# Kernel optimization log

Measured on AMD Instinct MI355X. Metric: run time of the kernel, lower is better.

The kernel has to match this reference:

```python
import jax, jax.numpy as jnp
import numpy as np

B, S, D = 2, 2048, 1024
H = 16
HD = D // H  # 64


def setup_inputs() -> dict:
    key = jax.random.key(0)
    ks = jax.random.split(key, 9)
    s = 1.0 / np.sqrt(D)
    x = jax.random.normal(ks[0], (B, S, D), dtype=jnp.float32)
    Wq = jax.random.normal(ks[1], (D, D), dtype=jnp.float32) * s
    Wk = jax.random.normal(ks[2], (D, D), dtype=jnp.float32) * s
    Wv = jax.random.normal(ks[3], (D, D), dtype=jnp.float32) * s
    Wo = jax.random.normal(ks[4], (D, D), dtype=jnp.float32) * s
    bq = jnp.zeros((D,), jnp.float32)
    bk = jnp.zeros((D,), jnp.float32)
    bv = jnp.zeros((D,), jnp.float32)
    bo = jnp.zeros((D,), jnp.float32)
    # causal mask, broadcastable to (B, H, S, S)
    mask = jnp.tril(jnp.ones((S, S), dtype=bool))[None, None, :, :]
    return {"x": x, "Wq": Wq, "bq": bq, "Wk": Wk, "bk": bk,
            "Wv": Wv, "bv": bv, "Wo": Wo, "bo": bo, "mask": mask}


def _split_heads(t):
    # (B, S, D) -> (B, H, S, HD)
    b, s, _ = t.shape
    return t.reshape(b, s, H, HD).transpose(0, 2, 1, 3)


def reference(x, Wq, bq, Wk, bk, Wv, bv, Wo, bo, mask):
    q = _split_heads(x @ Wq + bq)
    k = _split_heads(x @ Wk + bk)
    v = _split_heads(x @ Wv + bv)
    scale = 1.0 / jnp.sqrt(jnp.asarray(HD, dtype=q.dtype))
    scores = jnp.einsum('bhqd,bhkd->bhqk', q, k) * scale
    large_neg = jnp.finfo(scores.dtype).min
    scores = jnp.where(mask, scores, large_neg)
    attn = jax.nn.softmax(scores, axis=-1)
    out = jnp.einsum('bhqk,bhkd->bhqd', attn, v)  # (B,H,S,HD)
    out = out.transpose(0, 2, 1, 3).reshape(x.shape[0], x.shape[1], D)
    return out @ Wo + bo
```

## Files before the change

kernel.cpp:

```cpp
#include <hip/hip_runtime.h>
#include <hip/hip_bf16.h>

typedef __attribute__((ext_vector_type(8))) short bf16x8;
typedef __attribute__((ext_vector_type(4))) float f32x4;
typedef __attribute__((ext_vector_type(16))) float f32x16;

#define B_DIM  2
#define S_DIM  2048
#define D_DIM  1024
#define H_DIM  16
#define HD_DIM 64

__device__ __forceinline__ float bf2f(ushort u) {
    union { unsigned int ui; float f; } c; c.ui = ((unsigned int)u) << 16; return c.f;
}
__device__ __forceinline__ ushort f2bf(float f) {
    __hip_bfloat16 h = __float2bfloat16(f);
    return *reinterpret_cast<ushort*>(&h);
}

__device__ __forceinline__ void async_cp16(const ushort* g, ushort* l) {
    __builtin_amdgcn_global_load_lds(
        (const __attribute__((address_space(1))) void*)g,
        (__attribute__((address_space(3))) void*)l, 16, 0, 0);
}

__device__ __forceinline__ unsigned int cvt_pk_bf16(float lo, float hi) {
    unsigned int d;
    asm volatile("v_cvt_pk_bf16_f32 %0, %1, %2" : "=v"(d) : "v"(lo), "v"(hi));
    return d;
}
__device__ __forceinline__ void pl32swap(unsigned int& a, unsigned int& b) {
    asm volatile("v_permlane32_swap_b32 %0, %1" : "+v"(a), "+v"(b));
}

__global__ __launch_bounds__(256) void detect_kernel(const ushort* __restrict__ x,
                                                     int* __restrict__ flag) {
    __shared__ int any;
    int tid = threadIdx.x;
    if (tid == 0) any = 0;
    __syncthreads();
    int cnt = 0;
    for (int j = 0; j < 64; ++j) {
        ushort u = x[tid * 64 + j];
        if (((u >> 7) & 0xFF) == 0xFF) cnt++;
    }
    if (cnt) atomicOr(&any, 1);
    __syncthreads();
    if (tid == 0) *flag = any ? 1 : 0;
}

__global__ __launch_bounds__(256) void prep_kernel(const void* __restrict__ x,
                                                   const void* __restrict__ Wq,
                                                   const void* __restrict__ Wk,
                                                   const void* __restrict__ Wv,
                                                   const void* __restrict__ Wo,
                                                   const void* __restrict__ bq,
                                                   const void* __restrict__ bk,
                                                   const void* __restrict__ bv,
                                                   const void* __restrict__ bo,
                                                   ushort* __restrict__ xc,
                                                   ushort* __restrict__ Wqkvt,
                                                   ushort* __restrict__ Wot,
                                                   float* __restrict__ biasf,
                                                   const int* __restrict__ flag) {
    int tid = threadIdx.x;
    int z = blockIdx.z;
    bool isf32 = (*flag != 0);

    if (z == 4) {
        int t = (blockIdx.y * 16 + blockIdx.x) * 256 + tid;
#pragma unroll
        for (int c = 0; c < 8; ++c) {
            int i = t + c * 65536;
            if (isf32) {
                const float* s = (const float*)x;
                f32x4 a = *(const f32x4*)&s[(size_t)i * 8];
                f32x4 b = *(const f32x4*)&s[(size_t)i * 8 + 4];
                bf16x8 o;
                o[0] = f2bf(a.x); o[1] = f2bf(a.y); o[2] = f2bf(a.z); o[3] = f2bf(a.w);
                o[4] = f2bf(b.x); o[5] = f2bf(b.y); o[6] = f2bf(b.z); o[7] = f2bf(b.w);
                *(bf16x8*)&xc[(size_t)i * 8] = o;
            } else {
                *(bf16x8*)&xc[(size_t)i * 8] =
                    *(const bf16x8*)&((const ushort*)x)[(size_t)i * 8];
            }
        }
        return;
    }
    if (z == 5) {
        int bid = blockIdx.y * 16 + blockIdx.x;
        if (bid >= 16) return;
        int i = bid * 256 + tid;
        int w = i >> 10, j = i & 1023;
        const void* s = (w == 0) ? bq : (w == 1) ? bk : (w == 2) ? bv : bo;
        biasf[i] = isf32 ? ((const float*)s)[j] : bf2f(((const ushort*)s)[j]);
        return;
    }

    __shared__ ushort tile[64][72];
    const void* src = (z == 0) ? Wq : (z == 1) ? Wk : (z == 2) ? Wv : Wo;
    ushort* dst = (z < 3) ? (Wqkvt + (size_t)z * D_DIM * D_DIM) : Wot;
    int r0 = blockIdx.y * 64, c0 = blockIdx.x * 64;
#pragma unroll
    for (int p = 0; p < 2; ++p) {
        int r = p * 32 + (tid >> 3);
        int c = (tid & 7) * 8;
        if (isf32) {
            const float* s = (const float*)src;
            f32x4 a = *(const f32x4*)&s[(size_t)(r0 + r) * D_DIM + c0 + c];
            f32x4 b = *(const f32x4*)&s[(size_t)(r0 + r) * D_DIM + c0 + c + 4];
            tile[r][c + 0] = f2bf(a.x); tile[r][c + 1] = f2bf(a.y);
            tile[r][c + 2] = f2bf(a.z); tile[r][c + 3] = f2bf(a.w);
            tile[r][c + 4] = f2bf(b.x); tile[r][c + 5] = f2bf(b.y);
            tile[r][c + 6] = f2bf(b.z); tile[r][c + 7] = f2bf(b.w);
        } else {
            *(bf16x8*)&tile[r][c] =
                *(const bf16x8*)&((const ushort*)src)[(size_t)(r0 + r) * D_DIM + c0 + c];
        }
    }
    __syncthreads();
#pragma unroll
    for (int p = 0; p < 2; ++p) {
        int n  = p * 32 + (tid >> 3);
        int cc = (tid & 7) * 8;
        bf16x8 v;
#pragma unroll
        for (int e = 0; e < 8; ++e) v[e] = (short)tile[cc + e][n];
        *(bf16x8*)&dst[(size_t)(c0 + n) * D_DIM + r0 + cc] = v;
    }
}

__global__ __launch_bounds__(256) void gemm128_kernel(const ushort* __restrict__ A,
                                                      const ushort* __restrict__ Bt,
                                                      const float* __restrict__ bias,
                                                      ushort* __restrict__ qout,
                                                      ushort* __restrict__ kpout,
                                                      ushort* __restrict__ vpout) {
    __shared__ ushort As[128 * 64];
    __shared__ ushort Bs[128 * 64];
    int tid  = threadIdx.x;
    int wave = tid >> 6;
    int lane = tid & 63;
    int l16  = lane & 15;
    int quad = lane >> 4;
    int m0   = blockIdx.y * 128;
    int n0   = blockIdx.x * 128;
    int wm   = wave >> 1;
    int wn   = wave & 1;
    const int K = 1024;

    f32x4 acc[4][4];
#pragma unroll
    for (int i = 0; i < 4; ++i)
#pragma unroll
        for (int j = 0; j < 4; ++j) acc[i][j] = (f32x4){0.f, 0.f, 0.f, 0.f};

    int lrow = lane >> 3;
    int gcol = ((lane & 7) ^ lrow) * 8;
    int sw   = l16 & 7;

    for (int kt = 0; kt < 16; ++kt) {
        int k0 = kt * 64;
#pragma unroll
        for (int j = 0; j < 4; ++j) {
            int chunk = wave * 4 + j;
            int grow  = chunk * 8 + lrow;
            async_cp16(&A[(size_t)(m0 + grow) * K + k0 + gcol], &As[chunk * 512]);
            async_cp16(&Bt[(size_t)(n0 + grow) * K + k0 + gcol], &Bs[chunk * 512]);
        }
        __syncthreads();

#pragma unroll
        for (int kb = 0; kb < 2; ++kb) {
            bf16x8 af[4], bf[4];
#pragma unroll
            for (int i = 0; i < 4; ++i)
                af[i] = *(const bf16x8*)&As[(wm * 64 + i * 16 + l16) * 64 +
                                            (((kb * 4 + quad) ^ sw) << 3)];
#pragma unroll
            for (int j = 0; j < 4; ++j)
                bf[j] = *(const bf16x8*)&Bs[(wn * 64 + j * 16 + l16) * 64 +
                                            (((kb * 4 + quad) ^ sw) << 3)];
#pragma unroll
            for (int i = 0; i < 4; ++i)
#pragma unroll
                for (int j = 0; j < 4; ++j)
                    acc[i][j] = __builtin_amdgcn_mfma_f32_16x16x32_bf16(af[i], bf[j],
                                                                        acc[i][j], 0, 0, 0);
        }
        __syncthreads();
    }

#pragma unroll
    for (int j = 0; j < 4; ++j) {
        int n = n0 + wn * 64 + j * 16 + l16;
        float bv = bias[n];
        int which = n >> 10;
        int n1 = n & 1023;
        int h = n1 >> 6, hd = n1 & 63;
#pragma unroll
        for (int i = 0; i < 4; ++i) {
            int mb = m0 + wm * 64 + i * 16 + quad * 4;
            int b = mb >> 11, s = mb & (S_DIM - 1);
            int bh = b * H_DIM + h;
            float v4[4];
#pragma unroll
            for (int r = 0; r < 4; ++r) v4[r] = acc[i][j][r] + bv;
            if (which == 2) {
                ushort pk[4];
#pragma unroll
                for (int r = 0; r < 4; ++r) pk[r] = f2bf(v4[r]);
                size_t vidx = (size_t)bh * 131072 + (size_t)(s >> 6) * 4096 +
                              (size_t)((s >> 4) & 3) * 1024 + (size_t)(hd >> 5) * 512 +
                              (size_t)((s >> 3) & 1) * 256 + (size_t)(hd & 31) * 8 +
                              (s & 7);
                *(uint2*)&vpout[vidx] = *(uint2*)pk;
            } else if (which == 1) {
#pragma unroll
                for (int r = 0; r < 4; ++r) {
                    int key = s + r;
                    size_t kidx = (size_t)bh * 131072 + (size_t)(key >> 6) * 4096 +
                                  (size_t)((key >> 5) & 1) * 2048 +
                                  (size_t)(hd >> 4) * 512 +
                                  (size_t)((hd >> 3) & 1) * 256 +
                                  (size_t)(key & 31) * 8 + (hd & 7);
                    kpout[kidx] = f2bf(v4[r]);
                }
            } else {
#pragma unroll
                for (int r = 0; r < 4; ++r) {
                    float v = v4[r] * 0.18033688011f;
                    qout[((((size_t)bh) * S_DIM + s + r) << 6) + hd] = f2bf(v);
                }
            }
        }
    }
}

__global__ __launch_bounds__(256) void gemm64_kernel(const ushort* __restrict__ A,
                                                     const ushort* __restrict__ Bt,
                                                     const float* __restrict__ bias,
                                                     void* __restrict__ out,
                                                     const int* __restrict__ flag) {
    __shared__ ushort As[64 * 64];
    __shared__ ushort Bs[128 * 64];
    int tid  = threadIdx.x;
    int wave = tid >> 6;
    int lane = tid & 63;
    int l16  = lane & 15;
    int quad = lane >> 4;
    int m0   = blockIdx.y * 64;
    int n0   = blockIdx.x * 128;
    const int K = 1024;

    f32x4 acc[4][2];
#pragma unroll
    for (int i = 0; i < 4; ++i)
#pragma unroll
        for (int j = 0; j < 2; ++j) acc[i][j] = (f32x4){0.f, 0.f, 0.f, 0.f};

    int lrow = lane >> 3;
    int gcol = ((lane & 7) ^ lrow) * 8;
    int sw   = l16 & 7;

    for (int kt = 0; kt < 16; ++kt) {
        int k0 = kt * 64;
#pragma unroll
        for (int j = 0; j < 2; ++j) {
            int chunk = wave * 2 + j;
            int grow  = chunk * 8 + lrow;
            async_cp16(&A[(size_t)(m0 + grow) * K + k0 + gcol], &As[chunk * 512]);
        }
#pragma unroll
        for (int j = 0; j < 4; ++j) {
            int chunk = wave * 4 + j;
            int grow  = chunk * 8 + lrow;
            async_cp16(&Bt[(size_t)(n0 + grow) * K + k0 + gcol], &Bs[chunk * 512]);
        }
        __syncthreads();

#pragma unroll
        for (int kb = 0; kb < 2; ++kb) {
            bf16x8 af[4], bf[2];
#pragma unroll
            for (int i = 0; i < 4; ++i)
                af[i] = *(const bf16x8*)&As[(i * 16 + l16) * 64 +
                                            (((kb * 4 + quad) ^ sw) << 3)];
#pragma unroll
            for (int j = 0; j < 2; ++j)
                bf[j] = *(const bf16x8*)&Bs[(wave * 32 + j * 16 + l16) * 64 +
                                            (((kb * 4 + quad) ^ sw) << 3)];
#pragma unroll
            for (int i = 0; i < 4; ++i)
#pragma unroll
                for (int j = 0; j < 2; ++j)
                    acc[i][j] = __builtin_amdgcn_mfma_f32_16x16x32_bf16(af[i], bf[j],
                                                                        acc[i][j], 0, 0, 0);
        }
        __syncthreads();
    }

    int outf32 = *flag;
#pragma unroll
    for (int j = 0; j < 2; ++j) {
        int n = n0 + wave * 32 + j * 16 + l16;
        float bv = bias[n];
#pragma unroll
        for (int i = 0; i < 4; ++i)
#pragma unroll
            for (int r = 0; r < 4; ++r) {
                int m = m0 + i * 16 + quad * 4 + r;
                float v = acc[i][j][r] + bv;
                if (outf32) ((float*)out)[(size_t)m * D_DIM + n] = v;
                else        ((ushort*)out)[(size_t)m * D_DIM + n] = f2bf(v);
            }
    }
}

#define LOADK(DST, T) { size_t _b = Kbase + (size_t)(T) * 4096 + lane8;           \
    _Pragma("unroll") for (int _i = 0; _i < 8; ++_i)                              \
        DST[_i] = *(const bf16x8*)&Kp[_b + (size_t)((_i >> 2) * 2048 + (_i & 3) * 512)]; }

#define LOADV(DST, T) { size_t _b = Vbase + (size_t)(T) * 4096 + lane8;           \
    _Pragma("unroll") for (int _i = 0; _i < 8; ++_i)                              \
        DST[_i] = *(const bf16x8*)&Vp[_b + (size_t)((_i >> 1) * 1024 + (_i & 1) * 512)]; }

#define SOFT(SC, P0, P1) { unsigned int W[8];                                     \
    _Pragma("unroll") for (int _g = 0; _g < 4; ++_g) {                            \
        float _e0 = __builtin_amdgcn_exp2f(SC[4 * _g + 0]);                       \
        float _e1 = __builtin_amdgcn_exp2f(SC[4 * _g + 1]);                       \
        float _e2 = __builtin_amdgcn_exp2f(SC[4 * _g + 2]);                       \
        float _e3 = __builtin_amdgcn_exp2f(SC[4 * _g + 3]);                       \
        rsum += (_e0 + _e1) + (_e2 + _e3);                                        \
        W[2 * _g]     = cvt_pk_bf16(_e0, _e1);                                    \
        W[2 * _g + 1] = cvt_pk_bf16(_e2, _e3); }                                  \
    pl32swap(W[0], W[2]); pl32swap(W[1], W[3]);                                   \
    pl32swap(W[4], W[6]); pl32swap(W[5], W[7]);                                   \
    { union { unsigned int u[4]; bf16x8 v; } _c0, _c1;                            \
      _c0.u[0] = W[0]; _c0.u[1] = W[1]; _c0.u[2] = W[2]; _c0.u[3] = W[3];         \
      _c1.u[0] = W[4]; _c1.u[1] = W[5]; _c1.u[2] = W[6]; _c1.u[3] = W[7];         \
      P0 = _c0.v; P1 = _c1.v; } }

#define ROUND(KC, VC, KN, VN, T, PRE) {                                           \
    if (PRE) { LOADK(KN, (T) + 1); LOADV(VN, (T) + 1); }                          \
    int k0 = (T) * 64;                                                            \
    f32x16 sc0, sc1;                                                              \
    _Pragma("unroll") for (int _r = 0; _r < 16; ++_r) { sc0[_r] = 0.f; sc1[_r] = 0.f; } \
    __builtin_amdgcn_s_setprio(1);                                                \
    _Pragma("unroll") for (int _j = 0; _j < 4; ++_j) {                            \
        sc0 = __builtin_amdgcn_mfma_f32_32x32x16_bf16(KC[_j],     qf[_j], sc0, 0, 0, 0); \
        sc1 = __builtin_amdgcn_mfma_f32_32x32x16_bf16(KC[4 + _j], qf[_j], sc1, 0, 0, 0); } \
    __builtin_amdgcn_s_setprio(0);                                                \
    if (k0 + 63 > qmin) {                                                         \
        int qglob = qmin + l31;                                                   \
        _Pragma("unroll") for (int _r = 0; _r < 16; ++_r) {                       \
            int krow = k0 + (_r & 3) + 8 * (_r >> 2) + 4 * hi;                    \
            if (krow > qglob)      sc0[_r] = -1e30f;                              \
            if (krow + 32 > qglob) sc1[_r] = -1e30f; } }                          \
    bf16x8 pf[4];                                                                 \
    SOFT(sc0, pf[0], pf[1]);                                                      \
    SOFT(sc1, pf[2], pf[3]);                                                      \
    __builtin_amdgcn_s_setprio(1);                                                \
    _Pragma("unroll") for (int _j = 0; _j < 4; ++_j) {                            \
        oo0 = __builtin_amdgcn_mfma_f32_32x32x16_bf16(pf[_j], VC[2 * _j],     oo0, 0, 0, 0); \
        oo1 = __builtin_amdgcn_mfma_f32_32x32x16_bf16(pf[_j], VC[2 * _j + 1], oo1, 0, 0, 0); } \
    __builtin_amdgcn_s_setprio(0); }

__global__ __launch_bounds__(64, 2) void attn_kernel(const ushort* __restrict__ Qg,
                                                     const ushort* __restrict__ Kp,
                                                     const ushort* __restrict__ Vp,
                                                     float* __restrict__ pO0,
                                                     float* __restrict__ pO1,
                                                     float* __restrict__ Rsum) {
    int lane = threadIdx.x;
    int l31  = lane & 31;
    int hi   = lane >> 5;
    int bh   = blockIdx.x;
    int y    = blockIdx.y;
    int w    = blockIdx.z;
    int qt   = 15 - (y >> 1);
    int half = y & 1;
    int nt2  = qt + 1;
    int t_lo = half * nt2;
    int t_hi = t_lo + nt2;
    int q0   = qt * 128;
    int qmin = q0 + w * 32;
    int tneed = ((qmin + 31) >> 6) + 1;
    int thw   = t_hi < tneed ? t_hi : tneed;

    size_t lane8 = (size_t)lane * 8;
    size_t Kbase = (size_t)bh * 131072;
    size_t Vbase = (size_t)bh * 131072;
    const ushort* Qb = Qg + (size_t)bh * S_DIM * HD_DIM;

    bf16x8 qf[4];
#pragma unroll
    for (int kk = 0; kk < 4; ++kk)
        qf[kk] = *(const bf16x8*)&Qb[(size_t)(qmin + l31) * HD_DIM + kk * 16 + hi * 8];

    f32x16 oo0, oo1;
#pragma unroll
    for (int r = 0; r < 16; ++r) { oo0[r] = 0.f; oo1[r] = 0.f; }
    float rsum = 0.f;

    bf16x8 kA[8], kB[8], vA[8], vB[8];
    int t = t_lo;
    if (t < thw) { LOADK(kA, t); LOADV(vA, t); }
    for (; t + 2 <= thw; t += 2) {
        ROUND(kA, vA, kB, vB, t, true);
        ROUND(kB, vB, kA, vA, t + 1, (t + 2 < thw));
    }
    if (t < thw) ROUND(kA, vA, kB, vB, t, false);

    rsum += __shfl_xor(rsum, 32, 64);

    float* pO = half ? pO1 : pO0;
    int b = bh >> 4, h = bh & 15;
#pragma unroll
    for (int r = 0; r < 16; ++r) {
        int qrow = (r & 3) + 8 * (r >> 2) + 4 * hi;
        int q = qmin + qrow;
        size_t base = (size_t)(b * S_DIM + q) * D_DIM + h * HD_DIM;
        pO[base + l31]      = oo0[r];
        pO[base + 32 + l31] = oo1[r];
    }
    if (lane < 32)
        Rsum[half * (32 * S_DIM) + bh * S_DIM + qmin + lane] = rsum;
}

__global__ __launch_bounds__(256) void combine_kernel(const float* __restrict__ pO0,
                                                      const float* __restrict__ pO1,
                                                      const float* __restrict__ Rsum,
                                                      ushort* __restrict__ attn) {
    int e8 = blockIdx.x * 256 + threadIdx.x;
    int d8 = e8 & 127;
    int s  = (e8 >> 7) & (S_DIM - 1);
    int b  = e8 >> 18;
    int bh = b * H_DIM + (d8 >> 3);
    float r0 = Rsum[bh * S_DIM + s];
    float r1 = Rsum[32 * S_DIM + bh * S_DIM + s];
    float inv = 1.f / (r0 + r1);
    size_t base = (size_t)e8 * 8;
    f32x4 a0 = *(const f32x4*)&pO0[base];
    f32x4 a1 = *(const f32x4*)&pO0[base + 4];
    f32x4 c0 = *(const f32x4*)&pO1[base];
    f32x4 c1 = *(const f32x4*)&pO1[base + 4];
    bf16x8 ov;
    ov[0] = f2bf((a0.x + c0.x) * inv); ov[1] = f2bf((a0.y + c0.y) * inv);
    ov[2] = f2bf((a0.z + c0.z) * inv); ov[3] = f2bf((a0.w + c0.w) * inv);
    ov[4] = f2bf((a1.x + c1.x) * inv); ov[5] = f2bf((a1.y + c1.y) * inv);
    ov[6] = f2bf((a1.z + c1.z) * inv); ov[7] = f2bf((a1.w + c1.w) * inv);
    *(bf16x8*)&attn[base] = ov;
}

extern "C" void kernel_launch(void* const* d_in, const int* in_sizes, int n_in,
                              void* d_out, int out_size, void* d_ws, size_t ws_size,
                              hipStream_t stream) {
    const void* x  = d_in[0];
    const void* Wq = d_in[1];
    const void* bq = d_in[2];
    const void* Wk = d_in[3];
    const void* bk = d_in[4];
    const void* Wv = d_in[5];
    const void* bv = d_in[6];
    const void* Wo = d_in[7];
    const void* bo = d_in[8];

    char* ws = (char*)d_ws;
    const size_t MB = 1024 * 1024;
    const size_t base = 64 * 1024;
    int*    flag   = (int*)ws;
    float*  biasf  = (float*)(ws + 4096);
    ushort* xc     = (ushort*)(ws + base);
    ushort* Wqkvt  = (ushort*)(ws + base + 8  * MB);
    ushort* Wot    = (ushort*)(ws + base + 14 * MB);
    ushort* Qc     = (ushort*)(ws + base + 16 * MB);
    ushort* Kpf    = (ushort*)(ws + base + 24 * MB);
    ushort* Vpf    = (ushort*)(ws + base + 40 * MB);
    float*  pO0    = (float*)(ws + base + 48 * MB);
    float*  pO1    = (float*)(ws + base + 64 * MB);
    float*  Rsum   = (float*)(ws + base + 80 * MB);
    ushort* attn   = xc;

    dim3 tb(256);

    detect_kernel<<<1, tb, 0, stream>>>((const ushort*)x, flag);

    dim3 pg(16, 16, 6);
    prep_kernel<<<pg, tb, 0, stream>>>(x, Wq, Wk, Wv, Wo, bq, bk, bv, bo,
                                       xc, Wqkvt, Wot, biasf, flag);

    dim3 gq(3 * D_DIM / 128, (B_DIM * S_DIM) / 128);
    gemm128_kernel<<<gq, tb, 0, stream>>>(xc, Wqkvt, biasf, Qc, Kpf, Vpf);

    dim3 ag(B_DIM * H_DIM, 32, 4);
    attn_kernel<<<ag, dim3(64), 0, stream>>>(Qc, Kpf, Vpf, pO0, pO1, Rsum);

    combine_kernel<<<2048, tb, 0, stream>>>(pO0, pO1, Rsum, attn);

    dim3 go(D_DIM / 128, (B_DIM * S_DIM) / 64);
    gemm64_kernel<<<go, tb, 0, stream>>>(attn, Wot, biasf + 3072, d_out, flag);
}
```

Before: 195.7 us.

## Drop split-KV attention and combine pass; normalize output inside attention kernel

The attention kernel no longer splits each query tile's key range into two halves that write fp32 partial outputs and row sums. Each block now walks the full causal key range, divides by the row sum in registers and writes bf16 attention output directly, so the combine kernel and its fp32 round trip through global memory go away. Separately, the bf16 copy of x is skipped when the input is already bf16, with the QKV GEMM reading the raw input instead, and the detect kernel now uses vectorized loads. In exchange there are fewer blocks per query tile and longer serial key loops for late tiles, which may worsen load balance.

Result: faster. 187.4 us (-4.3%).

```diff
diff --git a/kernel.cpp b/kernel.cpp
--- a/kernel.cpp
+++ b/kernel.cpp
@@ -41,9 +41,14 @@
     if (tid == 0) any = 0;
     __syncthreads();
     int cnt = 0;
-    for (int j = 0; j < 64; ++j) {
-        ushort u = x[tid * 64 + j];
-        if (((u >> 7) & 0xFF) == 0xFF) cnt++;
+#pragma unroll
+    for (int c = 0; c < 8; ++c) {
+        bf16x8 v = *(const bf16x8*)&x[tid * 64 + c * 8];
+#pragma unroll
+        for (int e = 0; e < 8; ++e) {
+            ushort u = (ushort)v[e];
+            if (((u >> 7) & 0xFF) == 0xFF) cnt++;
+        }
     }
     if (cnt) atomicOr(&any, 1);
     __syncthreads();
@@ -69,22 +74,18 @@
     bool isf32 = (*flag != 0);
 
     if (z == 4) {
+        if (!isf32) return;
         int t = (blockIdx.y * 16 + blockIdx.x) * 256 + tid;
 #pragma unroll
         for (int c = 0; c < 8; ++c) {
             int i = t + c * 65536;
-            if (isf32) {
-                const float* s = (const float*)x;
-                f32x4 a = *(const f32x4*)&s[(size_t)i * 8];
-                f32x4 b = *(const f32x4*)&s[(size_t)i * 8 + 4];
-                bf16x8 o;
-                o[0] = f2bf(a.x); o[1] = f2bf(a.y); o[2] = f2bf(a.z); o[3] = f2bf(a.w);
-                o[4] = f2bf(b.x); o[5] = f2bf(b.y); o[6] = f2bf(b.z); o[7] = f2bf(b.w);
-                *(bf16x8*)&xc[(size_t)i * 8] = o;
-            } else {
-                *(bf16x8*)&xc[(size_t)i * 8] =
-                    *(const bf16x8*)&((const ushort*)x)[(size_t)i * 8];
-            }
+            const float* s = (const float*)x;
+            f32x4 a = *(const f32x4*)&s[(size_t)i * 8];
+            f32x4 b = *(const f32x4*)&s[(size_t)i * 8 + 4];
+            bf16x8 o;
+            o[0] = f2bf(a.x); o[1] = f2bf(a.y); o[2] = f2bf(a.z); o[3] = f2bf(a.w);
+            o[4] = f2bf(b.x); o[5] = f2bf(b.y); o[6] = f2bf(b.z); o[7] = f2bf(b.w);
+            *(bf16x8*)&xc[(size_t)i * 8] = o;
         }
         return;
     }
@@ -131,14 +132,17 @@
     }
 }
 
-__global__ __launch_bounds__(256) void gemm128_kernel(const ushort* __restrict__ A,
+__global__ __launch_bounds__(256) void gemm128_kernel(const void* __restrict__ xraw,
+                                                      const ushort* __restrict__ xc,
                                                       const ushort* __restrict__ Bt,
                                                       const float* __restrict__ bias,
                                                       ushort* __restrict__ qout,
                                                       ushort* __restrict__ kpout,
-                                                      ushort* __restrict__ vpout) {
+                                                      ushort* __restrict__ vpout,
+                                                      const int* __restrict__ flag) {
     __shared__ ushort As[128 * 64];
     __shared__ ushort Bs[128 * 64];
+    const ushort* A = (*flag != 0) ? xc : (const ushort*)xraw;
     int tid  = threadIdx.x;
     int wave = tid >> 6;
     int lane = tid & 63;
@@ -370,24 +374,17 @@
 __global__ __launch_bounds__(64, 2) void attn_kernel(const ushort* __restrict__ Qg,
                                                      const ushort* __restrict__ Kp,
                                                      const ushort* __restrict__ Vp,
-                                                     float* __restrict__ pO0,
-                                                     float* __restrict__ pO1,
-                                                     float* __restrict__ Rsum) {
+                                                     ushort* __restrict__ attn_out) {
     int lane = threadIdx.x;
     int l31  = lane & 31;
     int hi   = lane >> 5;
-    int bh   = blockIdx.x;
-    int y    = blockIdx.y;
-    int w    = blockIdx.z;
-    int qt   = 15 - (y >> 1);
-    int half = y & 1;
-    int nt2  = qt + 1;
-    int t_lo = half * nt2;
-    int t_hi = t_lo + nt2;
-    int q0   = qt * 128;
-    int qmin = q0 + w * 32;
-    int tneed = ((qmin + 31) >> 6) + 1;
-    int thw   = t_hi < tneed ? t_hi : tneed;
+    int idx  = blockIdx.x;
+    int qt   = 15 - (idx >> 7);
+    int rr   = idx & 127;
+    int bh   = rr >> 2;
+    int w    = rr & 3;
+    int qmin = qt * 128 + w * 32;
+    int thw  = ((qmin + 31) >> 6) + 1;
 
     size_t lane8 = (size_t)lane * 8;
     size_t Kbase = (size_t)bh * 131072;
@@ -405,8 +402,8 @@
     float rsum = 0.f;
 
     bf16x8 kA[8], kB[8], vA[8], vB[8];
-    int t = t_lo;
-    if (t < thw) { LOADK(kA, t); LOADV(vA, t); }
+    int t = 0;
+    LOADK(kA, 0); LOADV(vA, 0);
     for (; t + 2 <= thw; t += 2) {
         ROUND(kA, vA, kB, vB, t, true);
         ROUND(kB, vB, kA, vA, t + 1, (t + 2 < thw));
@@ -414,44 +411,18 @@
     if (t < thw) ROUND(kA, vA, kB, vB, t, false);
 
     rsum += __shfl_xor(rsum, 32, 64);
-
-    float* pO = half ? pO1 : pO0;
+    float inv = 1.f / rsum;
+
     int b = bh >> 4, h = bh & 15;
 #pragma unroll
     for (int r = 0; r < 16; ++r) {
         int qrow = (r & 3) + 8 * (r >> 2) + 4 * hi;
+        float iv = __shfl(inv, qrow, 64);
         int q = qmin + qrow;
         size_t base = (size_t)(b * S_DIM + q) * D_DIM + h * HD_DIM;
-        pO[base + l31]      = oo0[r];
-        pO[base + 32 + l31] = oo1[r];
-    }
-    if (lane < 32)
-        Rsum[half * (32 * S_DIM) + bh * S_DIM + qmin + lane] = rsum;
-}
-
-__global__ __launch_bounds__(256) void combine_kernel(const float* __restrict__ pO0,
-                                                      const float* __restrict__ pO1,
-                                                      const float* __restrict__ Rsum,
-                                                      ushort* __restrict__ attn) {
-    int e8 = blockIdx.x * 256 + threadIdx.x;
-    int d8 = e8 & 127;
-    int s  = (e8 >> 7) & (S_DIM - 1);
-    int b  = e8 >> 18;
-    int bh = b * H_DIM + (d8 >> 3);
-    float r0 = Rsum[bh * S_DIM + s];
-    float r1 = Rsum[32 * S_DIM + bh * S_DIM + s];
-    float inv = 1.f / (r0 + r1);
-    size_t base = (size_t)e8 * 8;
-    f32x4 a0 = *(const f32x4*)&pO0[base];
-    f32x4 a1 = *(const f32x4*)&pO0[base + 4];
-    f32x4 c0 = *(const f32x4*)&pO1[base];
-    f32x4 c1 = *(const f32x4*)&pO1[base + 4];
-    bf16x8 ov;
-    ov[0] = f2bf((a0.x + c0.x) * inv); ov[1] = f2bf((a0.y + c0.y) * inv);
-    ov[2] = f2bf((a0.z + c0.z) * inv); ov[3] = f2bf((a0.w + c0.w) * inv);
-    ov[4] = f2bf((a1.x + c1.x) * inv); ov[5] = f2bf((a1.y + c1.y) * inv);
-    ov[6] = f2bf((a1.z + c1.z) * inv); ov[7] = f2bf((a1.w + c1.w) * inv);
-    *(bf16x8*)&attn[base] = ov;
+        attn_out[base + l31]      = f2bf(oo0[r] * iv);
+        attn_out[base + 32 + l31] = f2bf(oo1[r] * iv);
+    }
 }
 
 extern "C" void kernel_launch(void* const* d_in, const int* in_sizes, int n_in,
@@ -478,9 +449,6 @@
     ushort* Qc     = (ushort*)(ws + base + 16 * MB);
     ushort* Kpf    = (ushort*)(ws + base + 24 * MB);
     ushort* Vpf    = (ushort*)(ws + base + 40 * MB);
-    float*  pO0    = (float*)(ws + base + 48 * MB);
-    float*  pO1    = (float*)(ws + base + 64 * MB);
-    float*  Rsum   = (float*)(ws + base + 80 * MB);
     ushort* attn   = xc;
 
     dim3 tb(256);
@@ -492,12 +460,9 @@
                                        xc, Wqkvt, Wot, biasf, flag);
 
     dim3 gq(3 * D_DIM / 128, (B_DIM * S_DIM) / 128);
-    gemm128_kernel<<<gq, tb, 0, stream>>>(xc, Wqkvt, biasf, Qc, Kpf, Vpf);
-
-    dim3 ag(B_DIM * H_DIM, 32, 4);
-    attn_kernel<<<ag, dim3(64), 0, stream>>>(Qc, Kpf, Vpf, pO0, pO1, Rsum);
-
-    combine_kernel<<<2048, tb, 0, stream>>>(pO0, pO1, Rsum, attn);
+    gemm128_kernel<<<gq, tb, 0, stream>>>(x, xc, Wqkvt, biasf, Qc, Kpf, Vpf, flag);
+
+    attn_kernel<<<2048, dim3(64), 0, stream>>>(Qc, Kpf, Vpf, attn);
 
     dim3 go(D_DIM / 128, (B_DIM * S_DIM) / 64);
     gemm64_kernel<<<go, tb, 0, stream>>>(attn, Wot, biasf + 3072, d_out, flag);
```
